# Performance work log

Hardware: AMD Instinct MI355X
Metric: run time of the kernel (lower is better)

## Reference

```python
import jax, jax.numpy as jnp
import numpy as np


def setup_inputs() -> dict:
    key = jax.random.key(0)
    ks = jax.random.split(key, 6)
    N, D, H, C = 4096, 2048, 512, 200
    feats = jax.random.normal(ks[0], (N, D), dtype=jnp.float32)
    targets = jax.random.randint(ks[1], (N,), 0, C)
    w1 = jax.random.normal(ks[2], (2 * D, H), dtype=jnp.float32) * 0.02
    b1 = jnp.zeros((H,), dtype=jnp.float32)
    w2 = jax.random.normal(ks[3], (H, D), dtype=jnp.float32) * 0.02
    b2 = jnp.zeros((D,), dtype=jnp.float32)
    wfc = jax.random.normal(ks[4], (D, C), dtype=jnp.float32) * 0.02
    bfc = jnp.zeros((C,), dtype=jnp.float32)
    return {"feats": feats, "targets": targets, "w1": w1, "b1": b1,
            "w2": w2, "b2": b2, "wfc": wfc, "bfc": bfc}


def _match_pair(feats, targets):
    # pairwise Euclidean distances (N x N)
    sq = jnp.sum(feats * feats, axis=1)
    d2 = sq[:, None] + sq[None, :] - 2.0 * (feats @ feats.T)
    dist = jnp.sqrt(jnp.maximum(d2, 0.0))
    same = targets[:, None] == targets[None, :]
    inf = jnp.asarray(jnp.inf, dist.dtype)
    # nearest same-class neighbor, skipping self (distance 0 is rank 0)
    m_intra = jnp.where(same, dist, inf)
    intras = jnp.argsort(m_intra, axis=1)[:, 1]
    # nearest different-class neighbor
    m_inter = jnp.where(same, inf, dist)
    inters = jnp.argmin(m_inter, axis=1)
    return feats[intras], feats[inters], targets[inters]


def reference(feats, targets, w1, b1, w2, b2, wfc, bfc):
    intra_feats, inter_feats, inter_labels = _match_pair(feats, targets)
    x_feat = jnp.concatenate([feats, feats], axis=0)           # 2N x D
    y_feat = jnp.concatenate([intra_feats, inter_feats], axis=0)
    # MLP (dropout inactive at eval)
    h = jnp.concatenate([x_feat, y_feat], axis=1) @ w1 + b1
    m_feat = h @ w2 + b2
    gate_x = jax.nn.sigmoid(m_feat * x_feat)
    gate_y = jax.nn.sigmoid(m_feat * y_feat)
    x_self = x_feat + x_feat * gate_x
    x_other = x_feat + x_feat * gate_y
    y_self = y_feat + y_feat * gate_y
    y_other = y_feat + y_feat * gate_x
    logit1_self = jax.nn.sigmoid(x_self @ wfc + bfc)
    logit1_other = jax.nn.sigmoid(x_other @ wfc + bfc)
    logit2_self = jax.nn.sigmoid(y_self @ wfc + bfc)
    logit2_other = jax.nn.sigmoid(y_other @ wfc + bfc)
    labels1 = jnp.concatenate([targets, targets], axis=0)
    labels2 = jnp.concatenate([targets, inter_labels], axis=0)
    return (logit1_self, logit1_other, logit2_self, logit2_other, labels1, labels2)
```

## Files before the change

### kernel.cpp

```cpp
#include <hip/hip_runtime.h>
#include <math.h>

#define N 4096
#define D 2048
#define H 512
#define C 200
#define NR 8192
#define LDH 40

typedef unsigned long long u64;
typedef unsigned int u32;
typedef float f32x4 __attribute__((ext_vector_type(4)));
typedef _Float16 f16x8 __attribute__((ext_vector_type(8)));
typedef _Float16 f16x4 __attribute__((ext_vector_type(4)));

__device__ __forceinline__ float sigm(float z) {
  return __builtin_amdgcn_rcpf(1.0f + __expf(-z));
}
__device__ __forceinline__ float bf2f(unsigned short u) { return __uint_as_float(((u32)u) << 16); }
__device__ __forceinline__ unsigned short f2bf(float x) {
  u32 u = __float_as_uint(x);
  return (unsigned short)((u + 0x7fffu + ((u >> 16) & 1u)) >> 16);
}

__device__ __forceinline__ void gll16(const _Float16* g, _Float16* l) {
  __builtin_amdgcn_global_load_lds(
      (const __attribute__((address_space(1))) u32*)g,
      (__attribute__((address_space(3))) u32*)l, 16, 0, 0);
}

__global__ __launch_bounds__(256) void kc_pack_k1(const float* __restrict__ f,
                                                  _Float16* __restrict__ hiP,
                                                  _Float16* __restrict__ loP,
                                                  float* __restrict__ sq,
                                                  u64* __restrict__ bi,
                                                  u64* __restrict__ be) {
  __shared__ float wsum[4];
  const int r = blockIdx.x;
  const int t = threadIdx.x;
  const int kb = t >> 2, slot = t & 3;
  const float* src = f + (size_t)r * D + t * 8;
  float4 v0 = *(const float4*)src;
  float4 v1 = *(const float4*)(src + 4);
  f16x8 hv, lv;
  const float xs[8] = {v0.x, v0.y, v0.z, v0.w, v1.x, v1.y, v1.z, v1.w};
  float s = 0.0f;
#pragma unroll
  for (int j = 0; j < 8; ++j) {
    const _Float16 h = (_Float16)xs[j];
    hv[j] = h;
    lv[j] = (_Float16)(xs[j] - (float)h);
    s += xs[j] * xs[j];
  }
  const size_t off = ((size_t)((r >> 7) * 64 + kb) * 128 + (r & 127)) * 32 +
                     ((slot ^ ((r >> 1) & 3)) << 3);
  *(f16x8*)(hiP + off) = hv;
  *(f16x8*)(loP + off) = lv;
  for (int o = 32; o > 0; o >>= 1) s += __shfl_down(s, o);
  if ((t & 63) == 0) wsum[t >> 6] = s;
  __syncthreads();
  if (t == 0) {
    sq[r] = wsum[0] + wsum[1] + wsum[2] + wsum[3];
    bi[r] = ~0ull; be[r] = ~0ull;
  }
}

__global__ void kc_T(const float* __restrict__ in, _Float16* __restrict__ out,
                     int R, int Cc) {
  __shared__ float t[32][33];
  const int c0 = blockIdx.x * 32, r0 = blockIdx.y * 32;
  for (int i = threadIdx.y; i < 32; i += 8)
    t[i][threadIdx.x] = in[(size_t)(r0 + i) * Cc + c0 + threadIdx.x];
  __syncthreads();
  for (int i = threadIdx.y; i < 32; i += 8)
    out[(size_t)(c0 + i) * R + r0 + threadIdx.x] = (_Float16)t[threadIdx.x][i];
}

__global__ __launch_bounds__(256) void kc_packW(const float* __restrict__ w,
                                                _Float16* __restrict__ wP,
                                                int Ncols, int KB) {
  __shared__ float t[32][132];
  const int tid = threadIdx.x;
  const int kb = blockIdx.x, nb = blockIdx.y;
#pragma unroll
  for (int it = 0; it < 4; ++it) {
    const int idx = it * 256 + tid;
    const int k = idx >> 5, nq = idx & 31;
    float4 v = *(const float4*)(w + (size_t)(kb * 32 + k) * Ncols + nb * 128 + nq * 4);
    t[k][nq * 4 + 0] = v.x; t[k][nq * 4 + 1] = v.y;
    t[k][nq * 4 + 2] = v.z; t[k][nq * 4 + 3] = v.w;
  }
  __syncthreads();
#pragma unroll
  for (int it = 0; it < 2; ++it) {
    const int idx = it * 256 + tid;
    const int n = idx >> 2, slot = idx & 3;
    f16x8 v;
#pragma unroll
    for (int j = 0; j < 8; ++j) v[j] = (_Float16)t[slot * 8 + j][n];
    *(f16x8*)(wP + ((size_t)(nb * KB + kb) * 128 + n) * 32 +
              ((slot ^ ((n >> 1) & 3)) << 3)) = v;
  }
}

__global__ __launch_bounds__(64) void kc_wfc(const float* __restrict__ wfc,
                                             _Float16* __restrict__ wfcP) {
  const int kc = blockIdx.x, nf = blockIdx.y, l = threadIdx.x;
  const int n = nf * 16 + (l & 15);
  const int k = kc * 32 + (l >> 4) * 8;
  f16x8 v;
#pragma unroll
  for (int j = 0; j < 8; ++j)
    v[j] = (n < C) ? (_Float16)wfc[(size_t)(k + j) * C + n] : (_Float16)0.0f;
  *(f16x8*)(wfcP + ((size_t)(kc * 14 + nf) * 64 + l) * 8) = v;
}

__global__ __launch_bounds__(256, 4) void k2_dist(
    const _Float16* __restrict__ fhiP, const _Float16* __restrict__ floP,
    const int* __restrict__ tgt, const float* __restrict__ sq,
    u64* __restrict__ bi, u64* __restrict__ be) {
  __shared__ __align__(16) _Float16 S[4][4096];
  __shared__ float sqi[128], sqj[128];
  __shared__ int ti[128], tj[128];
  __shared__ u64 Li[2][128], Lj[2][128];

  const int tid = threadIdx.x;
  const int bid = blockIdx.x;
  const int b = (bid & 7) * 66 + (bid >> 3);
  int bj = (int)((sqrtf(8.0f * (float)b + 1.0f) - 1.0f) * 0.5f);
  while ((bj + 1) * (bj + 2) / 2 <= b) ++bj;
  while (bj * (bj + 1) / 2 > b) --bj;
  const int bib = b - bj * (bj + 1) / 2;
  const int i0 = bib * 128, j0 = bj * 128;
  const bool diag = (i0 == j0);

  const int l = tid & 63;
  const int w = tid >> 6;
  const int wr = w >> 1, wc = w & 1;
  const int fr = l & 15, fg = l >> 4;
  const int pswz = ((fr >> 1) & 3) << 3;

  const _Float16* psrc = ((w & 1) ? floP : fhiP) +
                         ((size_t)((w < 2 ? bib : bj) * 64) * 4096) + l * 8;

  if (tid < 128) { sqi[tid] = sq[i0 + tid]; ti[tid] = tgt[i0 + tid]; }
  else { const int t = tid - 128; sqj[t] = sq[j0 + t]; tj[t] = tgt[j0 + t]; }
  ((u64*)Li)[tid] = ~0ull;
  ((u64*)Lj)[tid] = ~0ull;

  f32x4 acc[4][4] = {};

  for (int k = 0; k < 64; ++k) {
    {
      const _Float16* gsrc = psrc + (size_t)k * 4096;
      _Float16* ldst = &S[w][0];
#pragma unroll
      for (int ii = 0; ii < 8; ++ii) gll16(gsrc + ii * 512, ldst + ii * 512);
    }
    __syncthreads();
    f16x8 ah[4], al[4], bh[4], bl[4];
#pragma unroll
    for (int m = 0; m < 4; ++m) {
      const int off = (wr * 64 + m * 16 + fr) * 32 + ((fg << 3) ^ pswz);
      ah[m] = *(const f16x8*)&S[0][off];
      al[m] = *(const f16x8*)&S[1][off];
    }
#pragma unroll
    for (int n = 0; n < 4; ++n) {
      const int off = (wc * 64 + n * 16 + fr) * 32 + ((fg << 3) ^ pswz);
      bh[n] = *(const f16x8*)&S[2][off];
      bl[n] = *(const f16x8*)&S[3][off];
    }
#pragma unroll
    for (int m = 0; m < 4; ++m)
#pragma unroll
      for (int n = 0; n < 4; ++n) {
        acc[m][n] = __builtin_amdgcn_mfma_f32_16x16x32_f16(ah[m], bh[n], acc[m][n], 0, 0, 0);
        acc[m][n] = __builtin_amdgcn_mfma_f32_16x16x32_f16(ah[m], bl[n], acc[m][n], 0, 0, 0);
        acc[m][n] = __builtin_amdgcn_mfma_f32_16x16x32_f16(al[m], bh[n], acc[m][n], 0, 0, 0);
      }
    __syncthreads();
  }

#pragma unroll
  for (int m = 0; m < 4; ++m) {
#pragma unroll
    for (int reg = 0; reg < 4; ++reg) {
      const int row_l = wr * 64 + m * 16 + fg * 4 + reg;
      const float si = sqi[row_l];
      const int ci = ti[row_l];
      u64 ks = ~0ull, kd = ~0ull;
#pragma unroll
      for (int n = 0; n < 4; ++n) {
        const int col_l = wc * 64 + n * 16 + fr;
        const float d2 = si + sqj[col_l] - 2.0f * acc[m][n][reg];
        const u64 key = ((u64)__float_as_uint(d2) << 32) | (u32)(j0 + col_l);
        if (ci == tj[col_l]) {
          if (i0 + row_l != j0 + col_l) ks = key < ks ? key : ks;
        } else {
          kd = key < kd ? key : kd;
        }
      }
#pragma unroll
      for (int off = 1; off < 16; off <<= 1) {
        u64 o = __shfl_xor(ks, off); ks = o < ks ? o : ks;
        o = __shfl_xor(kd, off);     kd = o < kd ? o : kd;
      }
      if (fr == 0) {
        if (ks != ~0ull) atomicMin(&Li[0][row_l], ks);
        if (kd != ~0ull) atomicMin(&Li[1][row_l], kd);
      }
    }
  }
  if (!diag) {
#pragma unroll
    for (int n = 0; n < 4; ++n) {
      const int col_l = wc * 64 + n * 16 + fr;
      const float sj = sqj[col_l];
      const int cj = tj[col_l];
      u64 ks = ~0ull, kd = ~0ull;
#pragma unroll
      for (int m = 0; m < 4; ++m)
#pragma unroll
        for (int reg = 0; reg < 4; ++reg) {
          const int row_l = wr * 64 + m * 16 + fg * 4 + reg;
          const float d2 = sqi[row_l] + sj - 2.0f * acc[m][n][reg];
          const u64 key = ((u64)__float_as_uint(d2) << 32) | (u32)(i0 + row_l);
          if (ti[row_l] == cj) ks = key < ks ? key : ks;
          else                 kd = key < kd ? key : kd;
        }
#pragma unroll
      for (int off = 16; off < 64; off <<= 1) {
        u64 o = __shfl_xor(ks, off); ks = o < ks ? o : ks;
        o = __shfl_xor(kd, off);     kd = o < kd ? o : kd;
      }
      if (fg == 0) {
        if (ks != ~0ull) atomicMin(&Lj[0][col_l], ks);
        if (kd != ~0ull) atomicMin(&Lj[1][col_l], kd);
      }
    }
  }
  __syncthreads();
  if (tid < 128) {
    u64 v = Li[0][tid]; if (v != ~0ull) atomicMin(&bi[i0 + tid], v);
    v = Li[1][tid];     if (v != ~0ull) atomicMin(&be[i0 + tid], v);
  } else if (!diag) {
    const int t = tid - 128;
    u64 v = Lj[0][t]; if (v != ~0ull) atomicMin(&bi[j0 + t], v);
    v = Lj[1][t];     if (v != ~0ull) atomicMin(&be[j0 + t], v);
  }
}

__global__ __launch_bounds__(256) void k3_prep(const int* __restrict__ tgt,
                                               const u64* __restrict__ bi,
                                               const u64* __restrict__ be,
                                               int* __restrict__ iy,
                                               float* __restrict__ lab1,
                                               float* __restrict__ lab2) {
  const int r = blockIdx.x * 256 + threadIdx.x;
  if (r >= NR) return;
  if (r < N) {
    iy[r] = (int)(bi[r] & 0xffffffffull);
    const float t = (float)tgt[r];
    lab1[r] = t; lab2[r] = t;
  } else {
    const int s = r - N;
    const int j = (int)(be[s] & 0xffffffffull);
    iy[r] = j;
    lab1[r] = (float)tgt[s];
    lab2[r] = (float)tgt[j];
  }
}

__global__ __launch_bounds__(256, 4) void k4_h(const _Float16* __restrict__ fhiP,
                                               const _Float16* __restrict__ w1P,
                                               const float* __restrict__ b1,
                                               const int* __restrict__ iy,
                                               _Float16* __restrict__ hout) {
  __shared__ __align__(16) _Float16 As[2 * 2048];
  __shared__ __align__(16) _Float16 Bs[2 * 4096];
  __shared__ int iy_s[64];
  const int tid = threadIdx.x;
  const int bid = blockIdx.x;
  const int b = (bid & 7) * 64 + (bid >> 3);
  const int nIdx = b >> 7, mIdx = b & 127;
  const int r0 = mIdx * 64, n0 = nIdx * 128;
  if (tid < 64) iy_s[tid] = iy[r0 + tid];
  const int l = tid & 63, w = tid >> 6;
  const int fr = l & 15, fg = l >> 4;
  const int pswz = ((fr >> 1) & 3) << 3;
  f32x4 acc[4][2] = {};
  const int gr0 = r0 & (N - 1);
  const _Float16* paBase = fhiP + ((size_t)((gr0 >> 7) * 64) * 4096) + (gr0 & 127) * 32;

#define K4_MFMA()                                                                   \
  do {                                                                              \
    _Pragma("unroll") for (int p = 0; p < 2; ++p) {                                 \
      f16x8 a[4], bb[2];                                                            \
      _Pragma("unroll") for (int m = 0; m < 4; ++m)                                 \
        a[m] = *(const f16x8*)&As[p * 2048 + (m * 16 + fr) * 32 + ((fg << 3) ^ pswz)]; \
      _Pragma("unroll") for (int nf = 0; nf < 2; ++nf)                              \
        bb[nf] = *(const f16x8*)&Bs[p * 4096 + (w * 32 + nf * 16 + fr) * 32 +       \
                                    ((fg << 3) ^ pswz)];                            \
      _Pragma("unroll") for (int m = 0; m < 4; ++m)                                 \
        _Pragma("unroll") for (int nf = 0; nf < 2; ++nf)                            \
          acc[m][nf] = __builtin_amdgcn_mfma_f32_16x16x32_f16(a[m], bb[nf],         \
                                                              acc[m][nf], 0, 0, 0); \
    }                                                                               \
  } while (0)

  for (int ks = 0; ks < 32; ++ks) {
    const int kbA = ks * 2;
    __syncthreads();
    {
      const _Float16* pa = paBase + (size_t)kbA * 4096 + l * 8;
      const _Float16* pb = w1P + (size_t)(nIdx * 128 + kbA) * 4096 + l * 8;
#pragma unroll
      for (int cc = 0; cc < 6; ++cc) {
        const int c = w * 6 + cc;
        if (c < 8) {
          const int p = c >> 2, co = c & 3;
          gll16(pa + p * 4096 + co * 512, &As[p * 2048 + co * 512]);
        } else {
          const int cb = c - 8;
          gll16(pb + cb * 512, &Bs[cb * 512]);
        }
      }
    }
    __syncthreads();
    K4_MFMA();
  }
  for (int ks = 0; ks < 32; ++ks) {
    const int kbA = ks * 2;
    const int kbW = 64 + ks * 2;
    __syncthreads();
    {
      const _Float16* pb = w1P + (size_t)(nIdx * 128 + kbW) * 4096 + l * 8;
#pragma unroll
      for (int cc = 0; cc < 4; ++cc) {
        const int cb = w * 4 + cc;
        gll16(pb + cb * 512, &Bs[cb * 512]);
      }
    }
#pragma unroll
    for (int it = 0; it < 2; ++it) {
      const int idx = it * 256 + tid;
      const int row = idx >> 3, p = (idx >> 2) & 1, slot = idx & 3;
      const int gy = iy_s[row];
      const _Float16* src = fhiP +
          ((size_t)((gy >> 7) * 64 + kbA + p) * 128 + (gy & 127)) * 32 +
          ((slot ^ ((gy >> 1) & 3)) << 3);
      *(uint4*)&As[p * 2048 + row * 32 + ((slot ^ ((row >> 1) & 3)) << 3)] =
          *(const uint4*)src;
    }
    __syncthreads();
    K4_MFMA();
  }
#undef K4_MFMA

#pragma unroll
  for (int nf = 0; nf < 2; ++nf) {
    const int gcol = n0 + w * 32 + nf * 16 + fr;
    const float bias = b1[gcol];
#pragma unroll
    for (int m = 0; m < 4; ++m)
#pragma unroll
      for (int reg = 0; reg < 4; ++reg) {
        const int grow = r0 + m * 16 + fg * 4 + reg;
        hout[(size_t)grow * H + gcol] = (_Float16)(acc[m][nf][reg] + bias);
      }
  }
}

__global__ __launch_bounds__(256, 4) void k5_m(const _Float16* __restrict__ hbuf,
                                               const _Float16* __restrict__ w2T,
                                               const float* __restrict__ b2,
                                               unsigned short* __restrict__ mbuf) {
  __shared__ __align__(16) _Float16 As[128 * LDH], Bs[128 * LDH];
  const int tid = threadIdx.x;
  const int bid = blockIdx.x;
  const int b = (bid & 7) * 128 + (bid >> 3);
  const int n0 = (b & 15) * 128, r0 = (b >> 4) * 128;
  const int l = tid & 63, w = tid >> 6;
  const int wr = w >> 1, wc = w & 1, fr = l & 15, fg = l >> 4;
  f32x4 acc[4][4] = {};

  for (int k0 = 0; k0 < H; k0 += 32) {
    __syncthreads();
#pragma unroll
    for (int it = 0; it < 2; ++it) {
      const int c = it * 256 + tid;
      const int row = c >> 2, xc = c & 3;
      const int la = row * LDH + xc * 8;
      *(uint4*)&As[la] = *(const uint4*)(hbuf + (size_t)(r0 + row) * H + k0 + xc * 8);
      *(uint4*)&Bs[la] = *(const uint4*)(w2T + (size_t)(n0 + row) * H + k0 + xc * 8);
    }
    __syncthreads();
    f16x8 a[4], bb[4];
#pragma unroll
    for (int m = 0; m < 4; ++m) a[m] = *(const f16x8*)&As[(wr * 64 + m * 16 + fr) * LDH + fg * 8];
#pragma unroll
    for (int n = 0; n < 4; ++n) bb[n] = *(const f16x8*)&Bs[(wc * 64 + n * 16 + fr) * LDH + fg * 8];
#pragma unroll
    for (int m = 0; m < 4; ++m)
#pragma unroll
      for (int n = 0; n < 4; ++n)
        acc[m][n] = __builtin_amdgcn_mfma_f32_16x16x32_f16(a[m], bb[n], acc[m][n], 0, 0, 0);
  }
#pragma unroll
  for (int n = 0; n < 4; ++n) {
    const int gcol = n0 + wc * 64 + n * 16 + fr;
    const float bias = b2[gcol];
#pragma unroll
    for (int m = 0; m < 4; ++m)
#pragma unroll
      for (int reg = 0; reg < 4; ++reg) {
        const int grow = r0 + wr * 64 + m * 16 + fg * 4 + reg;
        mbuf[(size_t)grow * D + gcol] = f2bf(acc[m][n][reg] + bias);
      }
  }
}

__global__ __launch_bounds__(256, 2) void k6_logits(
    const float* __restrict__ feats, const unsigned short* __restrict__ mbuf,
    const int* __restrict__ iy, const _Float16* __restrict__ wfcP,
    const float* __restrict__ bfc, float* __restrict__ out) {
  __shared__ __align__(16) _Float16 As[2][64 * 64];
  __shared__ __align__(16) _Float16 Bs[2][14336];
  __shared__ int iy_s[16];
  const int tid = threadIdx.x;
  const int r0 = blockIdx.x * 16;
  const int l = tid & 63, v = tid >> 6;
  const int fr = l & 15, fg = l >> 4;
  if (tid < 16) iy_s[tid] = iy[r0 + tid];
  __syncthreads();
  const int rr = tid >> 4;
  const int kq = (tid & 15) << 2;
  const int rg = r0 + rr;
  const float* xptr = feats + (size_t)(rg & (N - 1)) * D;
  const float* yptr = feats + (size_t)iy_s[rr] * D;
  const unsigned short* mptr = mbuf + (size_t)rg * D;
  const int wsw = ((rr >> 1) & 3) | ((rr & 1) << 2);
  const int soff = ((((kq >> 3) ^ wsw)) << 3) + (kq & 7);
  const int rsw = (((fr >> 1) & 3) | ((fr & 1) << 2)) << 3;

  f32x4 acc[14] = {};

#define K6_GATES(buf, xv, yv, mv)                                     \
  do {                                                                \
    const float xs_[4] = {xv.x, xv.y, xv.z, xv.w};                    \
    const float ys_[4] = {yv.x, yv.y, yv.z, yv.w};                    \
    const unsigned short ms_[4] = {mv.x, mv.y, mv.z, mv.w};           \
    f16x4 a0, a1, a2, a3;                                             \
    _Pragma("unroll") for (int j = 0; j < 4; ++j) {                   \
      const float x = xs_[j], y = ys_[j], m = bf2f(ms_[j]);           \
      const float gx = sigm(m * x), gy = sigm(m * y);                 \
      a0[j] = (_Float16)(x * (1.0f + gx));                            \
      a1[j] = (_Float16)(x * (1.0f + gy));                            \
      a2[j] = (_Float16)(y * (1.0f + gy));                            \
      a3[j] = (_Float16)(y * (1.0f + gx));                            \
    }                                                                 \
    *(f16x4*)&As[buf][(rr)*64 + soff] = a0;                           \
    *(f16x4*)&As[buf][(16 + rr) * 64 + soff] = a1;                    \
    *(f16x4*)&As[buf][(32 + rr) * 64 + soff] = a2;                    \
    *(f16x4*)&As[buf][(48 + rr) * 64 + soff] = a3;                    \
  } while (0)

#define K6_STAGEB(k0n, buf)                                           \
  do {                                                                \
    const _Float16* src_ = wfcP + (size_t)((k0n) >> 5) * 7168;        \
    _Pragma("unroll") for (int c = 0; c < 7; ++c)                     \
      gll16(src_ + (c * 256 + tid) * 8, &Bs[buf][(c * 256 + tid) * 8]); \
  } while (0)

  {
    float4 xv = *(const float4*)(xptr + kq);
    float4 yv = *(const float4*)(yptr + kq);
    ushort4 mv = *(const ushort4*)(mptr + kq);
    K6_STAGEB(0, 0);
    K6_GATES(0, xv, yv, mv);
  }

  for (int k0 = 0; k0 < D; k0 += 64) {
    const int cur = (k0 >> 6) & 1;
    __syncthreads();
    float4 xv, yv; ushort4 mv;
    const bool more = (k0 + 64 < D);
    if (more) {
      xv = *(const float4*)(xptr + k0 + 64 + kq);
      yv = *(const float4*)(yptr + k0 + 64 + kq);
      mv = *(const ushort4*)(mptr + k0 + 64 + kq);
      K6_STAGEB(k0 + 64, cur ^ 1);
    }
#pragma unroll
    for (int ksl = 0; ksl < 2; ++ksl) {
      const f16x8 af =
          *(const f16x8*)&As[cur][(v * 16 + fr) * 64 + ((((ksl * 4 + fg) << 3)) ^ rsw)];
      const _Float16* bp = &Bs[cur][(size_t)ksl * 7168 + (size_t)l * 8];
#pragma unroll
      for (int nf = 0; nf < 14; ++nf) {
        const f16x8 bf = *(const f16x8*)(bp + nf * 512);
        acc[nf] = __builtin_amdgcn_mfma_f32_16x16x32_f16(af, bf, acc[nf], 0, 0, 0);
      }
    }
    if (more) K6_GATES(cur ^ 1, xv, yv, mv);
  }
#undef K6_GATES
#undef K6_STAGEB

  float* outv = out + (size_t)v * NR * C;
#pragma unroll
  for (int nf = 0; nf < 14; ++nf) {
    const int col = nf * 16 + fr;
    if (col < C) {
      const float bias = bfc[col];
#pragma unroll
      for (int reg = 0; reg < 4; ++reg) {
        const int row = r0 + fg * 4 + reg;
        outv[(size_t)row * C + col] = sigm(acc[nf][reg] + bias);
      }
    }
  }
}

extern "C" void kernel_launch(void* const* d_in, const int* in_sizes, int n_in,
                              void* d_out, int out_size, void* d_ws, size_t ws_size,
                              hipStream_t stream) {
  const float* feats = (const float*)d_in[0];
  const int*   tgt   = (const int*)d_in[1];
  const float* w1    = (const float*)d_in[2];
  const float* b1    = (const float*)d_in[3];
  const float* w2    = (const float*)d_in[4];
  const float* b2    = (const float*)d_in[5];
  const float* wfc   = (const float*)d_in[6];
  const float* bfc   = (const float*)d_in[7];
  float* out = (float*)d_out;

  char* ws = (char*)d_ws;
  float* sq = (float*)(ws);
  u64*   bi = (u64*)(ws + 16384);
  u64*   be = (u64*)(ws + 49152);
  int*   iy = (int*)(ws + 81920);
  _Float16* fhiP = (_Float16*)(ws + 131072);
  _Float16* floP = (_Float16*)(ws + 131072 + 16777216);
  unsigned short* mbuf = (unsigned short*)(ws + 131072);
  _Float16* w1P = (_Float16*)(ws + 33685504);
  _Float16* w2T = (_Float16*)(ws + 37879808);
  _Float16* hbuf = (_Float16*)(ws + 39976960);
  _Float16* wfcP = (_Float16*)(ws + 48365568);

  float* lab1 = out + (size_t)4 * NR * C;
  float* lab2 = lab1 + NR;

  kc_pack_k1<<<N, 256, 0, stream>>>(feats, fhiP, floP, sq, bi, be);
  kc_packW<<<dim3(128, 4), 256, 0, stream>>>(w1, w1P, 512, 128);
  kc_T<<<dim3(2048 / 32, 512 / 32), dim3(32, 8), 0, stream>>>(w2, w2T, 512, 2048);
  kc_wfc<<<dim3(64, 14), 64, 0, stream>>>(wfc, wfcP);
  k2_dist<<<528, 256, 0, stream>>>(fhiP, floP, tgt, sq, bi, be);
  k3_prep<<<NR / 256, 256, 0, stream>>>(tgt, bi, be, iy, lab1, lab2);
  k4_h<<<512, 256, 0, stream>>>(fhiP, w1P, b1, iy, hbuf);
  k5_m<<<1024, 256, 0, stream>>>(hbuf, w2T, b2, mbuf);
  k6_logits<<<NR / 16, 256, 0, stream>>>(feats, mbuf, iy, wfcP, bfc, out);
}
```

Baseline: 298.7 us.

## Double-buffer LDS tiles and switch distance GEMM to 32x32x16 MFMA

The pairwise-distance kernel now double-buffers its LDS tiles, issuing the global-to-LDS loads for the next K chunk before computing on the current one, which removes one barrier per iteration. It also moves from 16x16x32 to 32x32x16 MFMA tiles, with a matching change to the epilogue row/column mapping and shuffle reductions. LDS use doubles and occupancy hints drop from 4 to 2 blocks per CU, so there is less latency hiding from other resident blocks.

Measured after the change: 366.6 us. +22.7%, slower.

```diff
diff --git a/kernel.cpp b/kernel.cpp
--- a/kernel.cpp
+++ b/kernel.cpp
@@ -11,6 +11,7 @@
 typedef unsigned long long u64;
 typedef unsigned int u32;
 typedef float f32x4 __attribute__((ext_vector_type(4)));
+typedef float f32x16 __attribute__((ext_vector_type(16)));
 typedef _Float16 f16x8 __attribute__((ext_vector_type(8)));
 typedef _Float16 f16x4 __attribute__((ext_vector_type(4)));
 
@@ -115,11 +116,11 @@
   *(f16x8*)(wfcP + ((size_t)(kc * 14 + nf) * 64 + l) * 8) = v;
 }
 
-__global__ __launch_bounds__(256, 4) void k2_dist(
+__global__ __launch_bounds__(256, 2) void k2_dist(
     const _Float16* __restrict__ fhiP, const _Float16* __restrict__ floP,
     const int* __restrict__ tgt, const float* __restrict__ sq,
     u64* __restrict__ bi, u64* __restrict__ be) {
-  __shared__ __align__(16) _Float16 S[4][4096];
+  __shared__ __align__(16) _Float16 S[2][4][4096];
   __shared__ float sqi[128], sqj[128];
   __shared__ int ti[128], tj[128];
   __shared__ u64 Li[2][128], Lj[2][128];
@@ -137,63 +138,69 @@
   const int l = tid & 63;
   const int w = tid >> 6;
   const int wr = w >> 1, wc = w & 1;
-  const int fr = l & 15, fg = l >> 4;
-  const int pswz = ((fr >> 1) & 3) << 3;
+  const int c32 = l & 31, hi = l >> 5;
 
   const _Float16* psrc = ((w & 1) ? floP : fhiP) +
                          ((size_t)((w < 2 ? bib : bj) * 64) * 4096) + l * 8;
-
+#define STAGE(kk, d)                                              \
+  do {                                                            \
+    const _Float16* gsrc_ = psrc + (size_t)(kk)*4096;             \
+    _Float16* ldst_ = &S[d][w][0];                                \
+    _Pragma("unroll") for (int ii = 0; ii < 8; ++ii)              \
+        gll16(gsrc_ + ii * 512, ldst_ + ii * 512);                \
+  } while (0)
+
+  STAGE(0, 0);
   if (tid < 128) { sqi[tid] = sq[i0 + tid]; ti[tid] = tgt[i0 + tid]; }
   else { const int t = tid - 128; sqj[t] = sq[j0 + t]; tj[t] = tgt[j0 + t]; }
   ((u64*)Li)[tid] = ~0ull;
   ((u64*)Lj)[tid] = ~0ull;
-
-  f32x4 acc[4][4] = {};
+  __syncthreads();
+
+  f32x16 acc[2][2] = {};
 
   for (int k = 0; k < 64; ++k) {
-    {
-      const _Float16* gsrc = psrc + (size_t)k * 4096;
-      _Float16* ldst = &S[w][0];
-#pragma unroll
-      for (int ii = 0; ii < 8; ++ii) gll16(gsrc + ii * 512, ldst + ii * 512);
-    }
-    __syncthreads();
-    f16x8 ah[4], al[4], bh[4], bl[4];
-#pragma unroll
-    for (int m = 0; m < 4; ++m) {
-      const int off = (wr * 64 + m * 16 + fr) * 32 + ((fg << 3) ^ pswz);
-      ah[m] = *(const f16x8*)&S[0][off];
-      al[m] = *(const f16x8*)&S[1][off];
-    }
-#pragma unroll
-    for (int n = 0; n < 4; ++n) {
-      const int off = (wc * 64 + n * 16 + fr) * 32 + ((fg << 3) ^ pswz);
-      bh[n] = *(const f16x8*)&S[2][off];
-      bl[n] = *(const f16x8*)&S[3][off];
-    }
-#pragma unroll
-    for (int m = 0; m < 4; ++m)
-#pragma unroll
-      for (int n = 0; n < 4; ++n) {
-        acc[m][n] = __builtin_amdgcn_mfma_f32_16x16x32_f16(ah[m], bh[n], acc[m][n], 0, 0, 0);
-        acc[m][n] = __builtin_amdgcn_mfma_f32_16x16x32_f16(ah[m], bl[n], acc[m][n], 0, 0, 0);
-        acc[m][n] = __builtin_amdgcn_mfma_f32_16x16x32_f16(al[m], bh[n], acc[m][n], 0, 0, 0);
-      }
-    __syncthreads();
-  }
-
-#pragma unroll
-  for (int m = 0; m < 4; ++m) {
-#pragma unroll
-    for (int reg = 0; reg < 4; ++reg) {
-      const int row_l = wr * 64 + m * 16 + fg * 4 + reg;
+    const int cur = k & 1;
+    if (k < 63) STAGE(k + 1, cur ^ 1);
+#pragma unroll
+    for (int k16 = 0; k16 < 2; ++k16) {
+      f16x8 ah[2], al[2], bh[2], bl[2];
+#pragma unroll
+      for (int t = 0; t < 2; ++t) {
+        const int arow = wr * 64 + t * 32 + c32;
+        const int aoff = arow * 32 + ((((k16 << 1) | hi) ^ ((arow >> 1) & 3)) << 3);
+        ah[t] = *(const f16x8*)&S[cur][0][aoff];
+        al[t] = *(const f16x8*)&S[cur][1][aoff];
+        const int brow = wc * 64 + t * 32 + c32;
+        const int boff = brow * 32 + ((((k16 << 1) | hi) ^ ((brow >> 1) & 3)) << 3);
+        bh[t] = *(const f16x8*)&S[cur][2][boff];
+        bl[t] = *(const f16x8*)&S[cur][3][boff];
+      }
+#pragma unroll
+      for (int tm = 0; tm < 2; ++tm)
+#pragma unroll
+        for (int tn = 0; tn < 2; ++tn) {
+          acc[tm][tn] = __builtin_amdgcn_mfma_f32_32x32x16_f16(ah[tm], bh[tn], acc[tm][tn], 0, 0, 0);
+          acc[tm][tn] = __builtin_amdgcn_mfma_f32_32x32x16_f16(ah[tm], bl[tn], acc[tm][tn], 0, 0, 0);
+          acc[tm][tn] = __builtin_amdgcn_mfma_f32_32x32x16_f16(al[tm], bh[tn], acc[tm][tn], 0, 0, 0);
+        }
+    }
+    __syncthreads();
+  }
+#undef STAGE
+
+#pragma unroll
+  for (int tm = 0; tm < 2; ++tm) {
+#pragma unroll
+    for (int reg = 0; reg < 16; ++reg) {
+      const int row_l = wr * 64 + tm * 32 + (reg & 3) + 8 * (reg >> 2) + 4 * hi;
       const float si = sqi[row_l];
       const int ci = ti[row_l];
       u64 ks = ~0ull, kd = ~0ull;
 #pragma unroll
-      for (int n = 0; n < 4; ++n) {
-        const int col_l = wc * 64 + n * 16 + fr;
-        const float d2 = si + sqj[col_l] - 2.0f * acc[m][n][reg];
+      for (int tn = 0; tn < 2; ++tn) {
+        const int col_l = wc * 64 + tn * 32 + c32;
+        const float d2 = si + sqj[col_l] - 2.0f * acc[tm][tn][reg];
         const u64 key = ((u64)__float_as_uint(d2) << 32) | (u32)(j0 + col_l);
         if (ci == tj[col_l]) {
           if (i0 + row_l != j0 + col_l) ks = key < ks ? key : ks;
@@ -202,11 +209,11 @@
         }
       }
 #pragma unroll
-      for (int off = 1; off < 16; off <<= 1) {
+      for (int off = 1; off < 32; off <<= 1) {
         u64 o = __shfl_xor(ks, off); ks = o < ks ? o : ks;
         o = __shfl_xor(kd, off);     kd = o < kd ? o : kd;
       }
-      if (fr == 0) {
+      if (c32 == 0) {
         if (ks != ~0ull) atomicMin(&Li[0][row_l], ks);
         if (kd != ~0ull) atomicMin(&Li[1][row_l], kd);
       }
@@ -214,27 +221,24 @@
   }
   if (!diag) {
 #pragma unroll
-    for (int n = 0; n < 4; ++n) {
-      const int col_l = wc * 64 + n * 16 + fr;
+    for (int tn = 0; tn < 2; ++tn) {
+      const int col_l = wc * 64 + tn * 32 + c32;
       const float sj = sqj[col_l];
       const int cj = tj[col_l];
       u64 ks = ~0ull, kd = ~0ull;
 #pragma unroll
-      for (int m = 0; m < 4; ++m)
-#pragma unroll
-        for (int reg = 0; reg < 4; ++reg) {
-          const int row_l = wr * 64 + m * 16 + fg * 4 + reg;
-          const float d2 = sqi[row_l] + sj - 2.0f * acc[m][n][reg];
+      for (int tm = 0; tm < 2; ++tm)
+#pragma unroll
+        for (int reg = 0; reg < 16; ++reg) {
+          const int row_l = wr * 64 + tm * 32 + (reg & 3) + 8 * (reg >> 2) + 4 * hi;
+          const float d2 = sqi[row_l] + sj - 2.0f * acc[tm][tn][reg];
           const u64 key = ((u64)__float_as_uint(d2) << 32) | (u32)(i0 + row_l);
           if (ti[row_l] == cj) ks = key < ks ? key : ks;
           else                 kd = key < kd ? key : kd;
         }
-#pragma unroll
-      for (int off = 16; off < 64; off <<= 1) {
-        u64 o = __shfl_xor(ks, off); ks = o < ks ? o : ks;
-        o = __shfl_xor(kd, off);     kd = o < kd ? o : kd;
-      }
-      if (fg == 0) {
+      u64 o = __shfl_xor(ks, 32); ks = o < ks ? o : ks;
+      o = __shfl_xor(kd, 32);     kd = o < kd ? o : kd;
+      if (hi == 0) {
         if (ks != ~0ull) atomicMin(&Lj[0][col_l], ks);
         if (kd != ~0ull) atomicMin(&Lj[1][col_l], kd);
       }
```
